# Optimization experiments

Measured on AMD Instinct MI355X. Metric: run time of the kernel, lower is better.

The kernel has to match this reference:

```python
import jax, jax.numpy as jnp
import numpy as np
from jax import lax

GAMMA = 0.1


def setup_inputs() -> dict:
    key = jax.random.key(0)
    k1, k2 = jax.random.split(key)
    pred = jax.random.normal(k1, (64, 512), dtype=jnp.float32)
    target = jax.random.normal(k2, (64, 512), dtype=jnp.float32)
    return {"pred": pred, "target": target}


def _soft_dtw(pred, target, gamma=GAMMA):
    # pred, target: [B, L]
    B, L = pred.shape
    inf = jnp.float32(jnp.inf)
    # pairwise squared distances: [B, L, L]
    dist = (pred[:, :, None] - target[:, None, :]) ** 2

    def softmin3(r0, r1, r2):
        # -gamma * logsumexp(-r/gamma) over the 3 predecessors (stable)
        s = jnp.stack([r0, r1, r2], axis=-1)
        return -gamma * jax.nn.logsumexp(-s / gamma, axis=-1)

    # R[0, :] = [0, inf, inf, ...]  (row 0 of the (L+1)x(L+1) DP table)
    init_row = jnp.concatenate(
        [jnp.zeros((B, 1), jnp.float32), jnp.full((B, L), inf, jnp.float32)], axis=1
    )  # [B, L+1]

    def row_step(prev_row, d_row):
        # prev_row: R[i-1, :] of shape [B, L+1]; d_row: dist[:, i-1, :] of shape [B, L]
        r0s = prev_row[:, :-1].T  # R[i-1, j-1], [L, B]
        r1s = prev_row[:, 1:].T   # R[i-1, j],   [L, B]
        ds = d_row.T              # [L, B]

        def cell(r_left, inp):
            r0, r1, d = inp
            val = d + softmin3(r0, r1, r_left)
            return val, val

        _, vals = lax.scan(cell, jnp.full((B,), inf, jnp.float32), (r0s, r1s, ds))
        new_row = jnp.concatenate([jnp.full((B, 1), inf, jnp.float32), vals.T], axis=1)
        return new_row, None

    # scan over rows i = 1..L; dist reordered to [L, B, L]
    last_row, _ = lax.scan(row_step, init_row, jnp.swapaxes(dist, 0, 1))
    return last_row[:, -1].mean()  # R[:, L, L].mean()


def reference(pred, target):
    return _soft_dtw(pred, target)
```

## Files before the change

kernel.cpp:

```cpp
#include <hip/hip_runtime.h>

#define LSEQ 512
#define NB 64
#define NCHUNK 71

__device__ __forceinline__ float dpp_shr1(float x) {
  return __int_as_float(
      __builtin_amdgcn_update_dpp(0, __float_as_int(x), 0x138, 0xF, 0xF, false));
}
__device__ __forceinline__ float dpp_shl1(float x) {
  return __int_as_float(
      __builtin_amdgcn_update_dpp(0, __float_as_int(x), 0x130, 0xF, 0xF, false));
}

__device__ __forceinline__ float cell(float p, float tcur, float r0, float r1,
                                      float vprev) {
  const float diff = p - tcur;
  const float m = fminf(fminf(r0, r1), vprev);
  const float dm = __builtin_fmaf(diff, diff, m);
  const float md = __builtin_amdgcn_fmed3f(r0, r1, vprev);
  const float mx = fmaxf(fmaxf(r0, r1), vprev);
  const float e = 1.0f + (__builtin_amdgcn_exp2f(m - md) +
                          __builtin_amdgcn_exp2f(m - mx));
  return dm - __builtin_amdgcn_logf(e);
}

template <bool FULL>
__device__ __forceinline__ void chunk16(int cbase, const float* tgp,
                                        const float* ringP, float* ringW,
                                        float p, bool is_l0, bool is_wr,
                                        int lane, float& vprev, float& r0,
                                        float& tcur) {
  float tinj = tgp[(cbase + (lane & 15)) & 511];
  float rinj = ringP[(cbase + 1 + (lane & 15)) & 127];
  float vv[16];
#pragma unroll
  for (int u = 0; u < 16; ++u) {
    const float tsh = dpp_shr1(tcur);
    tcur = is_l0 ? tinj : tsh;
    const float vsh = dpp_shr1(vprev);
    const float r1 = is_l0 ? rinj : vsh;
    if (u < 15) {
      tinj = dpp_shl1(tinj);
      rinj = dpp_shl1(rinj);
    }
    const float v = cell(p, tcur, r0, r1, vprev);
    vv[u] = v;
    if (FULL) {
      vprev = v;
    } else {
      const int j = cbase + 1 + u - lane;
      vprev = (((unsigned)(j - 1)) < (unsigned)LSEQ) ? v : vprev;
    }
    r0 = r1;
  }

  if (is_wr) {
    const int wb = (cbase - 62) & 127;
#pragma unroll
    for (int k = 0; k < 8; ++k) {
      *(float2*)&ringW[(wb + 2 * k) & 127] =
          make_float2(vv[2 * k], vv[2 * k + 1]);
    }
  }
}

__global__ __launch_bounds__(512) void dtw_band(
    const float* __restrict__ pred, const float* __restrict__ target,
    float* __restrict__ part) {
  const int b = blockIdx.x;
  const int tid = threadIdx.x;
  const int w = tid >> 6;
  const int lane = tid & 63;
  const bool is_l0 = (lane == 0);
  const bool is_wr = (lane == 63) && (w < 7);

  __shared__ float tg[LSEQ];
  __shared__ float rings[8][128];

  const float SC = 3.79828146f;
  const float p = pred[b * LSEQ + tid] * SC;
  tg[tid] = target[b * LSEQ + tid] * SC;
  ((float*)rings)[tid] = INFINITY;
  ((float*)rings)[tid + 512] = INFINITY;

  const int lag = w * 80;
  const int cw0 = 5 * w;
  const float* __restrict__ ringP = rings[w == 0 ? 7 : w - 1];
  float* __restrict__ ringW = rings[w];

  float vprev = INFINITY;
  float r0 = (tid == 0) ? 0.0f : INFINITY;
  float tcur = 0.0f;

  for (int c = 0; c < NCHUNK; ++c) {
    __syncthreads();
    if (c < cw0 || c > cw0 + 35) continue;
    const int cbase = 16 * c - lag;
    if (c >= cw0 + 4 && c <= cw0 + 31)
      chunk16<true>(cbase, tg, ringP, ringW, p, is_l0, is_wr, lane, vprev, r0,
                    tcur);
    else
      chunk16<false>(cbase, tg, ringP, ringW, p, is_l0, is_wr, lane, vprev, r0,
                     tcur);
  }

  if (tid == LSEQ - 1) part[b] = vprev * 0.069314718f;
}

__global__ void dtw_reduce(const float* __restrict__ part,
                           float* __restrict__ out) {
  float v = part[threadIdx.x];
#pragma unroll
  for (int o = 32; o > 0; o >>= 1) v += __shfl_down(v, o);
  if (threadIdx.x == 0) out[0] = v * (1.0f / NB);
}

extern "C" void kernel_launch(void* const* d_in, const int* in_sizes, int n_in,
                              void* d_out, int out_size, void* d_ws,
                              size_t ws_size, hipStream_t stream) {
  const float* pred = (const float*)d_in[0];
  const float* target = (const float*)d_in[1];
  float* part = (float*)d_ws;

  dtw_band<<<NB, LSEQ, 0, stream>>>(pred, target, part);
  dtw_reduce<<<1, 64, 0, stream>>>(part, (float*)d_out);
}
```

Baseline: 102.1 us.

## Carry DP cells as deferred (exponent, mantissa) pairs to drop per-cell log

Each DP cell is now held as a pair (d, e) whose value is d - log2(e), so the log in the inner recurrence goes away. Each cell now needs three exp2 calls and multiplies instead of two exp2, one log and a med3. The mantissa is renormalized once per 16-cell chunk with bit manipulation so it cannot overflow. Lane-0 injection is folded into the DPP old-value operand instead of a select. The costs are a doubled ring buffer in shared memory (float2), extra registers, and an extra exp per cell.

```diff
diff --git a/kernel.cpp b/kernel.cpp
--- a/kernel.cpp
+++ b/kernel.cpp
@@ -4,64 +4,66 @@
 #define NB 64
 #define NCHUNK 71
 
-__device__ __forceinline__ float dpp_shr1(float x) {
-  return __int_as_float(
-      __builtin_amdgcn_update_dpp(0, __float_as_int(x), 0x138, 0xF, 0xF, false));
+__device__ __forceinline__ float dpp_shr1(float old, float x) {
+  return __int_as_float(__builtin_amdgcn_update_dpp(
+      __float_as_int(old), __float_as_int(x), 0x138, 0xF, 0xF, false));
 }
 __device__ __forceinline__ float dpp_shl1(float x) {
-  return __int_as_float(
-      __builtin_amdgcn_update_dpp(0, __float_as_int(x), 0x130, 0xF, 0xF, false));
-}
-
-__device__ __forceinline__ float cell(float p, float tcur, float r0, float r1,
-                                      float vprev) {
-  const float diff = p - tcur;
-  const float m = fminf(fminf(r0, r1), vprev);
-  const float dm = __builtin_fmaf(diff, diff, m);
-  const float md = __builtin_amdgcn_fmed3f(r0, r1, vprev);
-  const float mx = fmaxf(fmaxf(r0, r1), vprev);
-  const float e = 1.0f + (__builtin_amdgcn_exp2f(m - md) +
-                          __builtin_amdgcn_exp2f(m - mx));
-  return dm - __builtin_amdgcn_logf(e);
+  return __int_as_float(__builtin_amdgcn_update_dpp(
+      0, __float_as_int(x), 0x130, 0xF, 0xF, false));
 }
 
 template <bool FULL>
 __device__ __forceinline__ void chunk16(int cbase, const float* tgp,
-                                        const float* ringP, float* ringW,
-                                        float p, bool is_l0, bool is_wr,
-                                        int lane, float& vprev, float& r0,
-                                        float& tcur) {
+                                        const float2* ring2P, float2* ring2W,
+                                        float p, bool is_wr, int lane,
+                                        float& vd, float& ve, float& r0d,
+                                        float& r0e, float& tcur) {
+  const int eb = __float_as_int(ve);
+  const int E = (eb >> 23) - 127;
+  ve = __int_as_float((eb & 0x007FFFFF) | 0x3F800000);
+  vd -= (float)E;
+
   float tinj = tgp[(cbase + (lane & 15)) & 511];
-  float rinj = ringP[(cbase + 1 + (lane & 15)) & 127];
-  float vv[16];
+  const float2 rj = ring2P[(cbase + 1 + (lane & 15)) & 127];
+  float rdinj = rj.x, reinj = rj.y;
+
+  float2 vv[16];
 #pragma unroll
   for (int u = 0; u < 16; ++u) {
-    const float tsh = dpp_shr1(tcur);
-    tcur = is_l0 ? tinj : tsh;
-    const float vsh = dpp_shr1(vprev);
-    const float r1 = is_l0 ? rinj : vsh;
+    tcur = dpp_shr1(tinj, tcur);
+    const float r1d = dpp_shr1(rdinj, vd);
+    const float r1e = dpp_shr1(reinj, ve);
     if (u < 15) {
       tinj = dpp_shl1(tinj);
-      rinj = dpp_shl1(rinj);
+      rdinj = dpp_shl1(rdinj);
+      reinj = dpp_shl1(reinj);
     }
-    const float v = cell(p, tcur, r0, r1, vprev);
-    vv[u] = v;
+    const float diff = p - tcur;
+    const float M = fminf(fminf(r0d, r1d), vd);
+    const float t0 = __builtin_amdgcn_exp2f(M - r0d) * r0e;
+    const float t1 = __builtin_amdgcn_exp2f(M - r1d) * r1e;
+    const float tP = __builtin_amdgcn_exp2f(M - vd) * ve;
+    const float eN = (t0 + t1) + tP;
+    const float dN = __builtin_fmaf(diff, diff, M);
+    vv[u] = make_float2(dN, eN);
     if (FULL) {
-      vprev = v;
+      vd = dN;
+      ve = eN;
     } else {
       const int j = cbase + 1 + u - lane;
-      vprev = (((unsigned)(j - 1)) < (unsigned)LSEQ) ? v : vprev;
+      const bool act = ((unsigned)(j - 1)) < (unsigned)LSEQ;
+      vd = act ? dN : vd;
+      ve = act ? eN : ve;
     }
-    r0 = r1;
+    r0d = r1d;
+    r0e = r1e;
   }
 
   if (is_wr) {
     const int wb = (cbase - 62) & 127;
 #pragma unroll
-    for (int k = 0; k < 8; ++k) {
-      *(float2*)&ringW[(wb + 2 * k) & 127] =
-          make_float2(vv[2 * k], vv[2 * k + 1]);
-    }
+    for (int k = 0; k < 16; ++k) ring2W[(wb + k) & 127] = vv[k];
   }
 }
 
@@ -72,25 +74,28 @@
   const int tid = threadIdx.x;
   const int w = tid >> 6;
   const int lane = tid & 63;
-  const bool is_l0 = (lane == 0);
   const bool is_wr = (lane == 63) && (w < 7);
 
   __shared__ float tg[LSEQ];
-  __shared__ float rings[8][128];
+  __shared__ float2 rings2[8][128];
 
   const float SC = 3.79828146f;
   const float p = pred[b * LSEQ + tid] * SC;
   tg[tid] = target[b * LSEQ + tid] * SC;
-  ((float*)rings)[tid] = INFINITY;
-  ((float*)rings)[tid + 512] = INFINITY;
+  float* rf = (float*)rings2;
+  rf[tid] = (tid & 1) ? 1.0f : INFINITY;
+  rf[tid + 512] = (tid & 1) ? 1.0f : INFINITY;
+  rf[tid + 1024] = (tid & 1) ? 1.0f : INFINITY;
+  rf[tid + 1536] = (tid & 1) ? 1.0f : INFINITY;
 
   const int lag = w * 80;
   const int cw0 = 5 * w;
-  const float* __restrict__ ringP = rings[w == 0 ? 7 : w - 1];
-  float* __restrict__ ringW = rings[w];
+  const float2* __restrict__ ring2P = rings2[w == 0 ? 7 : w - 1];
+  float2* __restrict__ ring2W = rings2[w];
 
-  float vprev = INFINITY;
-  float r0 = (tid == 0) ? 0.0f : INFINITY;
+  float vd = INFINITY, ve = 1.0f;
+  float r0d = (tid == 0) ? 0.0f : INFINITY;
+  float r0e = 1.0f;
   float tcur = 0.0f;
 
   for (int c = 0; c < NCHUNK; ++c) {
@@ -98,14 +103,15 @@
     if (c < cw0 || c > cw0 + 35) continue;
     const int cbase = 16 * c - lag;
     if (c >= cw0 + 4 && c <= cw0 + 31)
-      chunk16<true>(cbase, tg, ringP, ringW, p, is_l0, is_wr, lane, vprev, r0,
-                    tcur);
+      chunk16<true>(cbase, tg, ring2P, ring2W, p, is_wr, lane, vd, ve, r0d,
+                    r0e, tcur);
     else
-      chunk16<false>(cbase, tg, ringP, ringW, p, is_l0, is_wr, lane, vprev, r0,
-                     tcur);
+      chunk16<false>(cbase, tg, ring2P, ring2W, p, is_wr, lane, vd, ve, r0d,
+                     r0e, tcur);
   }
 
-  if (tid == LSEQ - 1) part[b] = vprev * 0.069314718f;
+  if (tid == LSEQ - 1)
+    part[b] = (vd - __builtin_amdgcn_logf(ve)) * 0.069314718f;
 }
 
 __global__ void dtw_reduce(const float* __restrict__ part,
```

Result: slower. 108.4 us (+6.2%).
